# Kernel optimization log

Hardware: AMD Instinct MI355X
Metric: run time of the kernel (lower is better)

## Reference

```python
import jax, jax.numpy as jnp
import numpy as np

D_MODEL = 2048
NUM_HEADS = 16
HEAD_DIM = D_MODEL // NUM_HEADS  # 128
BASE = 10000.0


def rotate_half(x):
    x1, x2 = x[..., : x.shape[-1] // 2], x[..., x.shape[-1] // 2 :]
    return jnp.concatenate((-x2, x1), axis=-1)


def setup_inputs() -> dict:
    key = jax.random.key(0)
    ks = jax.random.split(key, 9)
    B, S, D = 2, 2048, D_MODEL
    s = 1.0 / np.sqrt(D)
    return {
        "x": jax.random.normal(ks[0], (B, S, D), dtype=jnp.float32),
        "Wq": jax.random.normal(ks[1], (D, D), dtype=jnp.float32) * s,
        "bq": jnp.zeros((D,), dtype=jnp.float32),
        "Wk": jax.random.normal(ks[2], (D, D), dtype=jnp.float32) * s,
        "bk": jnp.zeros((D,), dtype=jnp.float32),
        "Wv": jax.random.normal(ks[3], (D, D), dtype=jnp.float32) * s,
        "bv": jnp.zeros((D,), dtype=jnp.float32),
        "Wo": jax.random.normal(ks[4], (D, D), dtype=jnp.float32) * s,
        "bo": jnp.zeros((D,), dtype=jnp.float32),
    }


def reference(x, Wq, bq, Wk, bk, Wv, bv, Wo, bo):
    B, S, D = x.shape
    H, hd = NUM_HEADS, HEAD_DIM

    def proj(W, b):
        # nn.Linear: x @ W^T + b, then split heads -> [B, H, S, hd]
        return (x @ W.T + b).reshape(B, S, H, hd).transpose(0, 2, 1, 3)

    q = proj(Wq, bq)
    k = proj(Wk, bk)
    v = proj(Wv, bv)

    # Rotary embedding table (note: original applies cos()/sin() to a
    # tensor that already contains [sin(si), cos(si)] — reproduced faithfully).
    positions = jnp.arange(S, dtype=jnp.float32)
    inv_freq = 1.0 / (BASE ** (jnp.arange(0, hd, 2, dtype=jnp.float32) / hd))
    sinusoid = positions[:, None] * inv_freq[None, :]            # [S, hd/2]
    emb = jnp.concatenate((jnp.sin(sinusoid), jnp.cos(sinusoid)), axis=-1)  # [S, hd]
    cos_e = jnp.cos(emb)  # broadcast over [B, H, S, hd]
    sin_e = jnp.sin(emb)

    q_rot = q * cos_e + rotate_half(q) * sin_e
    k_rot = k * cos_e + rotate_half(k) * sin_e

    scale = 1.0 / jnp.sqrt(jnp.asarray(hd, dtype=x.dtype))
    attn = jnp.einsum("bhqd,bhkd->bhqk", q_rot, k_rot) * scale
    attn = jax.nn.softmax(attn, axis=-1)
    out = jnp.einsum("bhqk,bhkd->bhqd", attn, v)
    out = out.transpose(0, 2, 1, 3).reshape(B, S, D)
    return out @ Wo.T + bo
```

## Files before the change

### kernel.cpp

```cpp
#include <hip/hip_runtime.h>
#include <math.h>

#define D_MODEL 2048
#define NHEADS  16
#define HD      128
#define SEQ     2048
#define BATCH   2
#define SCALE   0.08838834764831845f
#define SMAX    20.0f

typedef __attribute__((ext_vector_type(8))) short short8;
typedef __attribute__((ext_vector_type(4))) float f32x4;

#define MFMA16(a,b,c) __builtin_amdgcn_mfma_f32_16x16x32_bf16((a),(b),(c),0,0,0)

__device__ __forceinline__ unsigned short f2bf(float x){
    unsigned u = __float_as_uint(x);
    return (unsigned short)((u + 0x7FFFu + ((u>>16)&1u)) >> 16);
}
__device__ __forceinline__ float bf2f(unsigned short h){ return __uint_as_float(((unsigned)h)<<16); }

__device__ __forceinline__ void async16(void* lds, const void* g){
    __builtin_amdgcn_global_load_lds((const __attribute__((address_space(1))) unsigned int*)g,
                                     (__attribute__((address_space(3))) unsigned int*)lds, 16, 0, 0);
}

__device__ __forceinline__ void split4(float4 v, ushort4* h, ushort4* l){
    h->x=f2bf(v.x); l->x=f2bf(v.x-bf2f(h->x));
    h->y=f2bf(v.y); l->y=f2bf(v.y-bf2f(h->y));
    h->z=f2bf(v.z); l->z=f2bf(v.z-bf2f(h->z));
    h->w=f2bf(v.w); l->w=f2bf(v.w-bf2f(h->w));
}

__global__ __launch_bounds__(256)
void prep_all(const float* __restrict__ x, const float* __restrict__ Wq,
              const float* __restrict__ Wk, const float* __restrict__ Wv,
              unsigned short* __restrict__ Xhi, unsigned short* __restrict__ Xlo,
              unsigned short* __restrict__ WqHi, unsigned short* __restrict__ WqLo,
              unsigned short* __restrict__ WkHi, unsigned short* __restrict__ WkLo,
              unsigned short* __restrict__ WvHi,
              float4* __restrict__ tab)
{
    const int b = blockIdx.x, t = threadIdx.x;
    if (b < 8192) {
        int i = b*256 + t;
        ushort4 h,l; split4(((const float4*)x)[i], &h, &l);
        ((ushort4*)Xhi)[i]=h; ((ushort4*)Xlo)[i]=l;
    } else if (b < 12288) {
        int i = (b-8192)*256 + t;
        ushort4 h,l; split4(((const float4*)Wq)[i], &h, &l);
        ((ushort4*)WqHi)[i]=h; ((ushort4*)WqLo)[i]=l;
    } else if (b < 16384) {
        int i = (b-12288)*256 + t;
        ushort4 h,l; split4(((const float4*)Wk)[i], &h, &l);
        ((ushort4*)WkHi)[i]=h; ((ushort4*)WkLo)[i]=l;
    } else if (b < 20480) {
        int i = (b-16384)*256 + t;
        ushort4 h,l; split4(((const float4*)Wv)[i], &h, &l);
        ((ushort4*)WvHi)[i]=h;
    } else {
        int i = (b-20480)*256 + t;
        int s = i >> 6, d = i & 63;
        float f = powf(10000.0f, -(float)d * (1.0f/64.0f));
        float sv = (float)s * f;
        float sn = sinf(sv), cs = cosf(sv);
        tab[i] = (float4){cosf(sn), sinf(sn), cosf(cs), sinf(cs)};
    }
}

__global__ __launch_bounds__(256)
void split_w(const float* __restrict__ src, unsigned short* __restrict__ hi,
             unsigned short* __restrict__ lo, int n4)
{
    int i = blockIdx.x*256 + threadIdx.x;
    if (i >= n4) return;
    ushort4 h,l; split4(((const float4*)src)[i], &h, &l);
    ((ushort4*)hi)[i]=h; ((ushort4*)lo)[i]=l;
}

template<bool THREE>
__device__ __forceinline__ void read_A(const unsigned short* Ah, const unsigned short* Al,
                                       short8 (&ah)[4], short8 (&al)[4],
                                       int wm, int quad, int l15)
{
#pragma unroll
    for (int mi=0;mi<4;mi++){
        int m = wm*64 + mi*16 + l15;
        int c = (quad ^ ((m>>1)&3))*8;
        ah[mi] = *(const short8*)&Ah[m*32 + c];
        al[mi] = *(const short8*)&Al[m*32 + c];
    }
}

template<bool THREE, int Q>
__device__ __forceinline__ void read_B(const unsigned short* Bh, const unsigned short* Bl,
                                       short8& bh, short8& bl, int wn, int quad, int l15)
{
    int n = wn*64 + Q*16 + l15;
    int c = (quad ^ ((n>>1)&3))*8;
    bh = *(const short8*)&Bh[n*32 + c];
    if constexpr (THREE) bl = *(const short8*)&Bl[n*32 + c];
    else                 bl = (short8){};
}

template<bool THREE, int Q>
__device__ __forceinline__ void col_mfma(const short8 (&ah)[4], const short8 (&al)[4],
                                         short8 bh, short8 bl, f32x4 (&acc)[4][4])
{
    __builtin_amdgcn_s_setprio(1);
    acc[0][Q] = MFMA16(ah[0], bh, acc[0][Q]);
    acc[1][Q] = MFMA16(ah[1], bh, acc[1][Q]);
    acc[2][Q] = MFMA16(ah[2], bh, acc[2][Q]);
    acc[3][Q] = MFMA16(ah[3], bh, acc[3][Q]);
    acc[0][Q] = MFMA16(al[0], bh, acc[0][Q]);
    acc[1][Q] = MFMA16(al[1], bh, acc[1][Q]);
    acc[2][Q] = MFMA16(al[2], bh, acc[2][Q]);
    acc[3][Q] = MFMA16(al[3], bh, acc[3][Q]);
    if constexpr (THREE) {
        acc[0][Q] = MFMA16(ah[0], bl, acc[0][Q]);
        acc[1][Q] = MFMA16(ah[1], bl, acc[1][Q]);
        acc[2][Q] = MFMA16(ah[2], bl, acc[2][Q]);
        acc[3][Q] = MFMA16(ah[3], bl, acc[3][Q]);
    }
    __builtin_amdgcn_s_setprio(0);
}

template<bool THREE>
__device__ __forceinline__ void gemm_core(const unsigned short* __restrict__ Agh,
                                          const unsigned short* __restrict__ Agl,
                                          const unsigned short* __restrict__ Bgh,
                                          const unsigned short* __restrict__ Bgl,
                                          unsigned short* lds, int m0, int n0,
                                          f32x4 (&acc)[4][4])
{
    const int t = threadIdx.x, w = t>>6, lane = t&63;
    const int quad = lane>>4, l15 = lane&15;
    const int wm = w>>1, wn = w&1;

    unsigned short *c0 = lds, *c1 = lds + 24576, *c2 = lds + 49152;

    auto stageA = [&](unsigned short* P, const unsigned short* SRC, int u, int kt2){
        int idx = t + u*512; int rw = idx>>2, sg = idx&3;
        int sgp = sg ^ ((rw>>1)&3);
        async16((char*)(P + rw*32 + sg*8), SRC + (size_t)(m0+rw)*2048 + kt2 + sgp*8);
    };
    auto stageB = [&](unsigned short* P, const unsigned short* SRC, int kt2){
        int rw = t>>2, sg = t&3; int sgp = sg ^ ((rw>>1)&3);
        async16((char*)(P + rw*32 + sg*8), SRC + (size_t)(n0+rw)*2048 + kt2 + sgp*8);
    };
    auto stage_tile = [&](unsigned short* P, int kt2){
        stageA(P,        Agh, 0, kt2);  stageA(P,        Agh, 1, kt2);
        stageA(P+8192,   Agl, 0, kt2);  stageA(P+8192,   Agl, 1, kt2);
        stageB(P+16384,  Bgh, kt2);
        if constexpr (THREE) stageB(P+20480, Bgl, kt2);
    };

    stage_tile(c0, 0);
    stage_tile(c1, 32);
    if constexpr (THREE) asm volatile("s_waitcnt vmcnt(6)" ::: "memory");
    else                 asm volatile("s_waitcnt vmcnt(5)" ::: "memory");
    __builtin_amdgcn_s_barrier();
    __builtin_amdgcn_sched_barrier(0);

    short8 ah[4], al[4], ahp[4], alp[4];
    short8 b0h, b0l, b1h, b1l, b2h, b2l, b3h, b3l, b0hp, b0lp;
    read_A<THREE>(c0, c0+8192, ah, al, wm, quad, l15);
    read_B<THREE,0>(c0+16384, c0+20480, b0h, b0l, wn, quad, l15);

    for (int kt = 0; kt < 64; ++kt) {
        const bool st  = (kt < 62);
        const int  kt2 = (kt+2)*32;

        read_B<THREE,1>(c0+16384, c0+20480, b1h, b1l, wn, quad, l15);
        if (st){ stageA(c2,       Agh, 0, kt2); stageA(c2,       Agh, 1, kt2); }
        col_mfma<THREE,0>(ah, al, b0h, b0l, acc);
        __builtin_amdgcn_sched_barrier(0);

        read_B<THREE,2>(c0+16384, c0+20480, b2h, b2l, wn, quad, l15);
        if (st){ stageA(c2+8192,  Agl, 0, kt2); stageA(c2+8192,  Agl, 1, kt2); }
        col_mfma<THREE,1>(ah, al, b1h, b1l, acc);
        __builtin_amdgcn_sched_barrier(0);

        read_B<THREE,3>(c0+16384, c0+20480, b3h, b3l, wn, quad, l15);
        if (st){ stageB(c2+16384, Bgh, kt2); }
        col_mfma<THREE,2>(ah, al, b2h, b2l, acc);
        __builtin_amdgcn_sched_barrier(0);

        if constexpr (THREE) { if (st) stageB(c2+20480, Bgl, kt2); }
        if (kt < 63) {
            __builtin_amdgcn_sched_barrier(0);
            asm volatile("s_waitcnt lgkmcnt(0)" ::: "memory");
            if (st) {
                if constexpr (THREE) asm volatile("s_waitcnt vmcnt(6)" ::: "memory");
                else                 asm volatile("s_waitcnt vmcnt(5)" ::: "memory");
            } else {
                asm volatile("s_waitcnt vmcnt(0)" ::: "memory");
            }
            __builtin_amdgcn_s_barrier();
            __builtin_amdgcn_sched_barrier(0);
            read_A<THREE>(c1, c1+8192, ahp, alp, wm, quad, l15);
            read_B<THREE,0>(c1+16384, c1+20480, b0hp, b0lp, wn, quad, l15);
            __builtin_amdgcn_sched_barrier(0);
            col_mfma<THREE,3>(ah, al, b3h, b3l, acc);
#pragma unroll
            for (int i=0;i<4;i++){ ah[i]=ahp[i]; al[i]=alp[i]; }
            b0h = b0hp; b0l = b0lp;
            unsigned short* tmp = c0; c0 = c1; c1 = c2; c2 = tmp;
        } else {
            col_mfma<THREE,3>(ah, al, b3h, b3l, acc);
        }
    }
}

__global__ __launch_bounds__(512,2)
void gemm_qk(const unsigned short* __restrict__ Xhi_g, const unsigned short* __restrict__ Xlo_g,
             const unsigned short* __restrict__ wsplit,
             const float* __restrict__ bq, const float* __restrict__ bk,
             const float4* __restrict__ tab,
             unsigned short* __restrict__ Qhi, unsigned short* __restrict__ Qlo,
             unsigned short* __restrict__ Khi, unsigned short* __restrict__ Klo)
{
    extern __shared__ unsigned short ldsm[];
    const int z = blockIdx.z;
    const unsigned short* Whi = wsplit + (size_t)z*8388608u;
    const unsigned short* Wlo = Whi + 4194304u;
    const int t = threadIdx.x, w = t>>6, lane = t&63;
    const int quad = lane>>4, l15 = lane&15;
    const int wm = w>>1, wn = w&1;
    const int m0 = blockIdx.y*256, n0 = blockIdx.x*128;

    f32x4 acc[4][4];
#pragma unroll
    for (int i=0;i<4;i++)
#pragma unroll
        for (int j=0;j<4;j++) acc[i][j] = (f32x4){0.f,0.f,0.f,0.f};

    gemm_core<true>(Xhi_g, Xlo_g, Whi, Wlo, ldsm, m0, n0, acc);
    __syncthreads();

    const float* bias = (z==0)?bq:bk;
#pragma unroll
    for (int ni=0;ni<4;ni++){
        float bv_ = bias[n0 + wn*64 + ni*16 + l15];
#pragma unroll
        for (int mi=0;mi<4;mi++){
            acc[mi][ni][0]+=bv_; acc[mi][ni][1]+=bv_; acc[mi][ni][2]+=bv_; acc[mi][ni][3]+=bv_;
        }
    }

    float* xch = (float*)ldsm;
    unsigned short* OHi = (z==0)?Qhi:Khi;
    unsigned short* OLo = (z==0)?Qlo:Klo;
    const float scl = (z==0)?SCALE:1.0f;
    const int h = blockIdx.x;
    const int b = m0>>11;
    const size_t bhbase = ((size_t)(b*16+h)*2048);

    if (wn == 0) {
#pragma unroll
        for (int mi=0;mi<4;mi++)
#pragma unroll
        for (int ni=2;ni<4;ni++)
#pragma unroll
        for (int r=0;r<4;r++)
            xch[(wm*64+mi*16+quad*4+r)*68 + (ni-2)*16+l15] = acc[mi][ni][r];
    } else {
#pragma unroll
        for (int mi=0;mi<4;mi++)
#pragma unroll
        for (int ni=0;ni<2;ni++)
#pragma unroll
        for (int r=0;r<4;r++)
            xch[(wm*64+mi*16+quad*4+r)*68 + 32 + ni*16+l15] = acc[mi][ni][r];
    }
    __syncthreads();

    if (wn == 0) {
#pragma unroll
        for (int ni2=0;ni2<2;ni2++){
            int d = ni2*16 + l15;
#pragma unroll
            for (int mi=0;mi<4;mi++)
#pragma unroll
            for (int r=0;r<4;r++){
                int ml = wm*64 + mi*16 + quad*4 + r;
                int s = (m0 + ml) & 2047;
                float4 tv = tab[s*64 + d];
                float c_lo = acc[mi][ni2][r];
                float c_hi = xch[ml*68 + 32 + d];
                float o1 = (c_lo*tv.x - c_hi*tv.y)*scl;
                float o2 = (c_hi*tv.z + c_lo*tv.w)*scl;
                size_t base = (bhbase + s)*128;
                unsigned short h1=f2bf(o1); OHi[base+d]=h1;    OLo[base+d]=f2bf(o1-bf2f(h1));
                unsigned short h2=f2bf(o2); OHi[base+64+d]=h2; OLo[base+64+d]=f2bf(o2-bf2f(h2));
            }
        }
    } else {
#pragma unroll
        for (int ni2=0;ni2<2;ni2++){
            int d = 32 + ni2*16 + l15;
#pragma unroll
            for (int mi=0;mi<4;mi++)
#pragma unroll
            for (int r=0;r<4;r++){
                int ml = wm*64 + mi*16 + quad*4 + r;
                int s = (m0 + ml) & 2047;
                float4 tv = tab[s*64 + d];
                float c_lo = xch[ml*68 + (d-32)];
                float c_hi = acc[mi][ni2+2][r];
                float o1 = (c_lo*tv.x - c_hi*tv.y)*scl;
                float o2 = (c_hi*tv.z + c_lo*tv.w)*scl;
                size_t base = (bhbase + s)*128;
                unsigned short h1=f2bf(o1); OHi[base+d]=h1;    OLo[base+d]=f2bf(o1-bf2f(h1));
                unsigned short h2=f2bf(o2); OHi[base+64+d]=h2; OLo[base+64+d]=f2bf(o2-bf2f(h2));
            }
        }
    }
}

__global__ __launch_bounds__(512,2)
void gemm_v(const unsigned short* __restrict__ Xhi_g, const unsigned short* __restrict__ Xlo_g,
            const unsigned short* __restrict__ WvHi,
            const float* __restrict__ bv, unsigned short* __restrict__ Vt)
{
    extern __shared__ unsigned short ldsm[];
    const int t = threadIdx.x, w = t>>6, lane = t&63;
    const int quad = lane>>4, l15 = lane&15;
    const int wm = w>>1, wn = w&1;
    const int m0 = blockIdx.y*256, n0 = blockIdx.x*128;

    f32x4 acc[4][4];
#pragma unroll
    for (int i=0;i<4;i++)
#pragma unroll
        for (int j=0;j<4;j++) acc[i][j] = (f32x4){0.f,0.f,0.f,0.f};

    gemm_core<false>(Xhi_g, Xlo_g, WvHi, nullptr, ldsm, m0, n0, acc);
    __syncthreads();

#pragma unroll
    for (int ni=0;ni<4;ni++){
        float bv_ = bv[n0 + wn*64 + ni*16 + l15];
#pragma unroll
        for (int mi=0;mi<4;mi++){
            acc[mi][ni][0]+=bv_; acc[mi][ni][1]+=bv_; acc[mi][ni][2]+=bv_; acc[mi][ni][3]+=bv_;
        }
    }

    unsigned short* vb = ldsm;
#pragma unroll
    for (int mi=0;mi<4;mi++)
#pragma unroll
    for (int ni=0;ni<4;ni++)
#pragma unroll
    for (int r=0;r<4;r++){
        int d  = wn*64 + ni*16 + l15;
        int ml = wm*64 + mi*16 + quad*4 + r;
        vb[d*264 + ml] = f2bf(acc[mi][ni][r]);
    }
    __syncthreads();

    const int b = m0>>11, s0 = m0&2047, h = blockIdx.x;
    unsigned short* vdst = Vt + (size_t)(b*16+h)*128*2048;
    const int dr = t>>2, part = (t&3)*64;
#pragma unroll
    for (int j=0;j<8;j++){
        uint4 v = *(const uint4*)&vb[dr*264 + part + j*8];
        *(uint4*)(vdst + (size_t)dr*2048 + s0 + part + j*8) = v;
    }
}

__global__ __launch_bounds__(512,2)
void gemm_o(const unsigned short* __restrict__ Ahi_g, const unsigned short* __restrict__ Alo_g,
            const unsigned short* __restrict__ Whi_g, const unsigned short* __restrict__ Wlo_g,
            const float* __restrict__ bias, float* __restrict__ out)
{
    extern __shared__ unsigned short ldsm[];
    const int t = threadIdx.x, w = t>>6, lane = t&63;
    const int quad = lane>>4, l15 = lane&15;
    const int wm = w>>1, wn = w&1;
    const int m0 = blockIdx.y*256, n0 = blockIdx.x*128;

    f32x4 acc[4][4];
#pragma unroll
    for (int i=0;i<4;i++)
#pragma unroll
        for (int j=0;j<4;j++) acc[i][j] = (f32x4){0.f,0.f,0.f,0.f};

    gemm_core<true>(Ahi_g, Alo_g, Whi_g, Wlo_g, ldsm, m0, n0, acc);

#pragma unroll
    for (int ni=0;ni<4;ni++){
        int n = n0 + wn*64 + ni*16 + l15;
        float bv_ = bias[n];
#pragma unroll
        for (int mi=0;mi<4;mi++)
#pragma unroll
        for (int r=0;r<4;r++){
            int m = m0 + wm*64 + mi*16 + quad*4 + r;
            out[(size_t)m*2048 + n] = acc[mi][ni][r] + bv_;
        }
    }
}

__global__ __launch_bounds__(256,2)
void flash_mfma(const unsigned short* __restrict__ Qhi, const unsigned short* __restrict__ Qlo,
                const unsigned short* __restrict__ Khi, const unsigned short* __restrict__ Klo,
                const unsigned short* __restrict__ Vt,
                unsigned short* __restrict__ Ohi, unsigned short* __restrict__ Olo)
{
    const int t=threadIdx.x, w=t>>6, lane=t&63, quad=lane>>4, l15=lane&15;
    const int bh = blockIdx.y, qt = blockIdx.x;

    __shared__ __align__(16) unsigned short sm[32768];
    unsigned short* Ps = sm + 24576 + w*2048;

    short8 qf[2][2][4];
    const size_t qrow = (size_t)bh*2048 + qt*128 + w*32;
#pragma unroll
    for (int mb=0;mb<2;mb++){
        size_t r = qrow + mb*16 + l15;
#pragma unroll
        for (int kc=0;kc<4;kc++){
            qf[0][mb][kc] = *(const short8*)(Qhi + r*128 + kc*32 + quad*8);
            qf[1][mb][kc] = *(const short8*)(Qlo + r*128 + kc*32 + quad*8);
        }
    }

    f32x4 O[2][8];
#pragma unroll
    for (int mb=0;mb<2;mb++)
#pragma unroll
        for (int nb=0;nb<8;nb++) O[mb][nb]=(f32x4){0.f,0.f,0.f,0.f};
    float lrow[2][4];
#pragma unroll
    for (int mb=0;mb<2;mb++)
#pragma unroll
        for (int r=0;r<4;r++) lrow[mb][r]=0.f;

    const char* KhiB = (const char*)(Khi + (size_t)bh*2048*128);
    const char* KloB = (const char*)(Klo + (size_t)bh*2048*128);
    const unsigned short* VtB = Vt + (size_t)bh*128*2048;
    char* smb = (char*)sm;

    for (int kt=0; kt<2048; kt+=64) {
#pragma unroll
        for (int i=0;i<4;i++){
            int o16 = t + 256*i;
            int krow = o16>>4, kc = o16&15;
            int kcp = kc ^ (krow&15);
            async16(smb + i*4096 + t*16,         KhiB + (size_t)kt*256 + krow*256 + kcp*16);
            async16(smb + 16384 + i*4096 + t*16, KloB + (size_t)kt*256 + krow*256 + kcp*16);
            int d = (t>>3) + i*32, c = t&7;
            int cp = c ^ (d&7);
            async16(smb + 32768 + i*4096 + t*16, VtB + (size_t)d*2048 + kt + cp*8);
        }
        __syncthreads();

        f32x4 S[2][4];
#pragma unroll
        for (int mb=0;mb<2;mb++)
#pragma unroll
            for (int nb=0;nb<4;nb++) S[mb][nb]=(f32x4){0.f,0.f,0.f,0.f};
#pragma unroll
        for (int kc=0;kc<4;kc++)
#pragma unroll
        for (int nb=0;nb<4;nb++){
            int m = nb*16+l15;
            int c = ((kc*4+quad) ^ (m&15))*8;
            short8 kh = *(const short8*)&sm[m*128 + c];
            short8 kl = *(const short8*)&sm[8192 + m*128 + c];
#pragma unroll
            for (int mb=0;mb<2;mb++){
                S[mb][nb] = MFMA16(qf[0][mb][kc], kh, S[mb][nb]);
                S[mb][nb] = MFMA16(qf[1][mb][kc], kh, S[mb][nb]);
                S[mb][nb] = MFMA16(qf[0][mb][kc], kl, S[mb][nb]);
            }
        }

#pragma unroll
        for (int mb=0;mb<2;mb++)
#pragma unroll
        for (int nb=0;nb<4;nb++)
#pragma unroll
        for (int r=0;r<4;r++){
            float p = __expf(S[mb][nb][r] - SMAX);
            lrow[mb][r] += p;
            int q = mb*16 + quad*4 + r;
            int c = nb*16 + l15;
            Ps[q*64 + (((c>>3)^(q&7))<<3) + (c&7)] = f2bf(p);
        }

#pragma unroll
        for (int kc2=0;kc2<2;kc2++){
            short8 pf0 = *(const short8*)&Ps[(l15)*64      + (((kc2*4+quad)^(l15&7))<<3)];
            short8 pf1 = *(const short8*)&Ps[(16+l15)*64   + (((kc2*4+quad)^(l15&7))<<3)];
#pragma unroll
            for (int nb=0;nb<8;nb++){
                int d = nb*16+l15;
                int c = ((kc2*4+quad) ^ (d&7))*8;
                short8 vf = *(const short8*)&sm[16384 + d*64 + c];
                O[0][nb] = MFMA16(pf0, vf, O[0][nb]);
                O[1][nb] = MFMA16(pf1, vf, O[1][nb]);
            }
        }
        __syncthreads();
    }

#pragma unroll
    for (int mb=0;mb<2;mb++)
#pragma unroll
        for (int d=1;d<16;d<<=1)
#pragma unroll
            for (int r=0;r<4;r++) lrow[mb][r] += __shfl_xor(lrow[mb][r], d);

    const int b = bh>>4, h = bh&15;
#pragma unroll
    for (int mb=0;mb<2;mb++)
#pragma unroll
    for (int nb=0;nb<8;nb++)
#pragma unroll
    for (int r=0;r<4;r++){
        float v = O[mb][nb][r] / lrow[mb][r];
        int qg = qt*128 + w*32 + mb*16 + quad*4 + r;
        size_t base = ((size_t)(b*2048 + qg))*2048 + h*128 + nb*16 + l15;
        unsigned short hh = f2bf(v);
        Ohi[base]=hh; Olo[base]=f2bf(v-bf2f(hh));
    }
}

extern "C" void kernel_launch(void* const* d_in, const int* in_sizes, int n_in,
                              void* d_out, int out_size, void* d_ws, size_t ws_size,
                              hipStream_t stream)
{
    (void)in_sizes; (void)n_in; (void)out_size; (void)ws_size;
    const float* x  = (const float*)d_in[0];
    const float* Wq = (const float*)d_in[1];
    const float* bq = (const float*)d_in[2];
    const float* Wk = (const float*)d_in[3];
    const float* bk = (const float*)d_in[4];
    const float* Wv = (const float*)d_in[5];
    const float* bv = (const float*)d_in[6];
    const float* Wo = (const float*)d_in[7];
    const float* bo = (const float*)d_in[8];
    float* out = (float*)d_out;

    unsigned short* wsB = (unsigned short*)d_ws;
    unsigned short* C0  = wsB + 20971520u;
    unsigned short* Qhi = C0;
    unsigned short* Qlo = C0 + 8388608u;
    unsigned short* Khi = C0 + 16777216u;
    unsigned short* Klo = C0 + 25165824u;
    unsigned short* Vt  = C0 + 33554432u;
    float4* tab = (float4*)(wsB + 62914560u);

    unsigned short* Xhi = (unsigned short*)d_out;
    unsigned short* Xlo = Xhi + 8388608u;

    static bool attr_done = false;
    if (!attr_done) {
        (void)hipFuncSetAttribute(reinterpret_cast<const void*>(&gemm_qk),
                                  hipFuncAttributeMaxDynamicSharedMemorySize, 147456);
        (void)hipFuncSetAttribute(reinterpret_cast<const void*>(&gemm_v),
                                  hipFuncAttributeMaxDynamicSharedMemorySize, 147456);
        (void)hipFuncSetAttribute(reinterpret_cast<const void*>(&gemm_o),
                                  hipFuncAttributeMaxDynamicSharedMemorySize, 147456);
        attr_done = true;
    }

    prep_all<<<20992,256,0,stream>>>(x, Wq, Wk, Wv,
                                     Xhi, Xlo,
                                     wsB,            wsB+4194304u,
                                     wsB+8388608u,   wsB+12582912u,
                                     wsB+16777216u,  tab);

    gemm_qk<<<dim3(16,16,2),512,147456,stream>>>(Xhi, Xlo, wsB, bq, bk, tab,
                                                 Qhi, Qlo, Khi, Klo);
    gemm_v <<<dim3(16,16),  512,147456,stream>>>(Xhi, Xlo, wsB+16777216u, bv, Vt);

    unsigned short* Ohi = wsB;
    unsigned short* Olo = wsB + 8388608u;
    flash_mfma<<<dim3(16,32),256,0,stream>>>(Qhi,Qlo,Khi,Klo,Vt, Ohi, Olo);

    unsigned short* WoHi = C0;
    unsigned short* WoLo = C0 + 4194304u;
    split_w<<<4096,256,0,stream>>>(Wo, WoHi, WoLo, 1048576);

    gemm_o<<<dim3(16,16),512,147456,stream>>>(Ohi, Olo, WoHi, WoLo, bo, out);
}
```

Measured before the change: 635.8 us.

## Rewrite QK projection GEMM with 256x256 tiles and shuffle-based rotary epilogue

Replaces the shared triple-buffered gemm_core for the Q/K projection with a dedicated kernel using 256x256 block tiles (8x4 MFMA tiles per wave) and double-buffered LDS. The B (weight) rows are permuted on load so that rotary pair partners d and d+64 land in adjacent lanes, letting the epilogue use __shfl_xor instead of an LDS exchange and extra syncthreads. This halves the grid and increases operand reuse per block, at the cost of a simpler pipeline with a full vmcnt(0) wait each k-step, higher register pressure from 128 accumulator floats, and 128KB LDS at 2 blocks/CU.

```diff
diff --git a/kernel.cpp b/kernel.cpp
--- a/kernel.cpp
+++ b/kernel.cpp
@@ -78,10 +78,146 @@
     ((ushort4*)hi)[i]=h; ((ushort4*)lo)[i]=l;
 }
 
+__global__ __launch_bounds__(512,2)
+void gemm_qk(const unsigned short* __restrict__ Xhi_g, const unsigned short* __restrict__ Xlo_g,
+             const unsigned short* __restrict__ wsplit,
+             const float* __restrict__ bq, const float* __restrict__ bk,
+             const float4* __restrict__ tab,
+             unsigned short* __restrict__ Qhi, unsigned short* __restrict__ Qlo,
+             unsigned short* __restrict__ Khi, unsigned short* __restrict__ Klo)
+{
+    extern __shared__ unsigned short ldsm[];
+    const int z = blockIdx.z;
+    const unsigned short* Whi = wsplit + (size_t)z*8388608u;
+    const unsigned short* Wlo = Whi + 4194304u;
+    const int t = threadIdx.x, w = t>>6, lane = t&63;
+    const int quad = lane>>4, l15 = lane&15;
+    const int wm = w>>2, wn = w&3;
+    const int m0 = blockIdx.y*256, n0 = blockIdx.x*256;
+
+    unsigned short *c0 = ldsm, *c1 = ldsm + 32768;
+
+    f32x4 acc[8][4];
+#pragma unroll
+    for (int i=0;i<8;i++)
+#pragma unroll
+        for (int j=0;j<4;j++) acc[i][j] = (f32x4){0.f,0.f,0.f,0.f};
+
+    auto stage_tile = [&](unsigned short* P, int kt){
+#pragma unroll
+        for (int u=0; u<2; ++u){
+            int idx = t + u*512, rw = idx>>2, sg = idx&3;
+            int sgp = sg ^ ((rw>>1)&3);
+            async16((char*)(P + rw*32 + sg*8), Xhi_g + (size_t)(m0+rw)*2048 + kt + sgp*8);
+        }
+#pragma unroll
+        for (int u=0; u<2; ++u){
+            int idx = t + u*512, rw = idx>>2, sg = idx&3;
+            int sgp = sg ^ ((rw>>1)&3);
+            async16((char*)(P + 8192 + rw*32 + sg*8), Xlo_g + (size_t)(m0+rw)*2048 + kt + sgp*8);
+        }
+#pragma unroll
+        for (int u=0; u<2; ++u){
+            int idx = t + u*512, rw = idx>>2, sg = idx&3;
+            int sgp = sg ^ ((rw>>1)&3);
+            int wrow = n0 + ((rw>>7)<<7) + ((rw&127)>>1) + (rw&1)*64;
+            async16((char*)(P + 16384 + rw*32 + sg*8), Whi + (size_t)wrow*2048 + kt + sgp*8);
+        }
+#pragma unroll
+        for (int u=0; u<2; ++u){
+            int idx = t + u*512, rw = idx>>2, sg = idx&3;
+            int sgp = sg ^ ((rw>>1)&3);
+            int wrow = n0 + ((rw>>7)<<7) + ((rw&127)>>1) + (rw&1)*64;
+            async16((char*)(P + 24576 + rw*32 + sg*8), Wlo + (size_t)wrow*2048 + kt + sgp*8);
+        }
+    };
+
+    stage_tile(c0, 0);
+
+    for (int kt = 0; kt < 64; ++kt) {
+        asm volatile("s_waitcnt vmcnt(0)" ::: "memory");
+        __builtin_amdgcn_s_barrier();
+        __builtin_amdgcn_sched_barrier(0);
+
+        if (kt < 63) stage_tile(c1, (kt+1)*32);
+
+        const unsigned short* Ah = c0;
+        const unsigned short* Al = c0 + 8192;
+        const unsigned short* Bh = c0 + 16384;
+        const unsigned short* Bl = c0 + 24576;
+
+        short8 bh[4], bl[4];
+#pragma unroll
+        for (int ni=0;ni<4;ni++){
+            int n = wn*64 + ni*16 + l15;
+            int c = (quad ^ ((n>>1)&3))*8;
+            bh[ni] = *(const short8*)&Bh[n*32 + c];
+            bl[ni] = *(const short8*)&Bl[n*32 + c];
+        }
+
+        __builtin_amdgcn_s_setprio(1);
+#pragma unroll
+        for (int mi=0;mi<8;mi++){
+            int m = wm*128 + mi*16 + l15;
+            int c = (quad ^ ((m>>1)&3))*8;
+            short8 ah = *(const short8*)&Ah[m*32 + c];
+            short8 al = *(const short8*)&Al[m*32 + c];
+            acc[mi][0] = MFMA16(ah, bh[0], acc[mi][0]);
+            acc[mi][1] = MFMA16(ah, bh[1], acc[mi][1]);
+            acc[mi][2] = MFMA16(ah, bh[2], acc[mi][2]);
+            acc[mi][3] = MFMA16(ah, bh[3], acc[mi][3]);
+            acc[mi][0] = MFMA16(al, bh[0], acc[mi][0]);
+            acc[mi][1] = MFMA16(al, bh[1], acc[mi][1]);
+            acc[mi][2] = MFMA16(al, bh[2], acc[mi][2]);
+            acc[mi][3] = MFMA16(al, bh[3], acc[mi][3]);
+            acc[mi][0] = MFMA16(ah, bl[0], acc[mi][0]);
+            acc[mi][1] = MFMA16(ah, bl[1], acc[mi][1]);
+            acc[mi][2] = MFMA16(ah, bl[2], acc[mi][2]);
+            acc[mi][3] = MFMA16(ah, bl[3], acc[mi][3]);
+        }
+        __builtin_amdgcn_s_setprio(0);
+
+        asm volatile("s_waitcnt lgkmcnt(0)" ::: "memory");
+        __builtin_amdgcn_sched_barrier(0);
+        unsigned short* tmp = c0; c0 = c1; c1 = tmp;
+    }
+
+    unsigned short* OHi = (z==0)?Qhi:Khi;
+    unsigned short* OLo = (z==0)?Qlo:Klo;
+    const float* bias = (z==0)?bq:bk;
+    const float scl = (z==0)?SCALE:1.0f;
+    const int head_g = blockIdx.x*2 + (wn>>1);
+    const int jbase  = (wn&1)*64;
+    const int odd    = l15 & 1;
+
+#pragma unroll
+    for (int ni=0;ni<4;ni++){
+        int j = jbase + ni*16 + l15;
+        int d = j>>1;
+        float bv_ = bias[head_g*128 + d + odd*64];
+        int dcol = odd ? (64 + d) : d;
+#pragma unroll
+        for (int mi=0;mi<8;mi++)
+#pragma unroll
+        for (int r=0;r<4;r++){
+            int gm = m0 + wm*128 + mi*16 + quad*4 + r;
+            int b  = gm >> 11, s = gm & 2047;
+            float v = acc[mi][ni][r] + bv_;
+            float p = __shfl_xor(v, 1);
+            float4 tv = tab[s*64 + d];
+            float o = odd ? (v*tv.z + p*tv.w)*scl
+                          : (v*tv.x - p*tv.y)*scl;
+            size_t base = (((size_t)(b*16 + head_g))*2048 + s)*128 + dcol;
+            unsigned short hh = f2bf(o);
+            OHi[base] = hh; OLo[base] = f2bf(o - bf2f(hh));
+        }
+    }
+}
+
 template<bool THREE>
-__device__ __forceinline__ void read_A(const unsigned short* Ah, const unsigned short* Al,
-                                       short8 (&ah)[4], short8 (&al)[4],
-                                       int wm, int quad, int l15)
+__device__ __forceinline__ void read_A3(const unsigned short* Ah, const unsigned short* Al,
+                                        short8 (&ah)[4], short8 (&al)[4],
+                                        int wm, int quad, int l15)
 {
 #pragma unroll
     for (int mi=0;mi<4;mi++){
@@ -93,8 +229,8 @@
 }
 
 template<bool THREE, int Q>
-__device__ __forceinline__ void read_B(const unsigned short* Bh, const unsigned short* Bl,
-                                       short8& bh, short8& bl, int wn, int quad, int l15)
+__device__ __forceinline__ void read_B3(const unsigned short* Bh, const unsigned short* Bl,
+                                        short8& bh, short8& bl, int wn, int quad, int l15)
 {
     int n = wn*64 + Q*16 + l15;
     int c = (quad ^ ((n>>1)&3))*8;
@@ -104,8 +240,8 @@
 }
 
 template<bool THREE, int Q>
-__device__ __forceinline__ void col_mfma(const short8 (&ah)[4], const short8 (&al)[4],
-                                         short8 bh, short8 bl, f32x4 (&acc)[4][4])
+__device__ __forceinline__ void col_mfma3(const short8 (&ah)[4], const short8 (&al)[4],
+                                          short8 bh, short8 bl, f32x4 (&acc)[4][4])
 {
     __builtin_amdgcn_s_setprio(1);
     acc[0][Q] = MFMA16(ah[0], bh, acc[0][Q]);
@@ -126,12 +262,12 @@
 }
 
 template<bool THREE>
-__device__ __forceinline__ void gemm_core(const unsigned short* __restrict__ Agh,
-                                          const unsigned short* __restrict__ Agl,
-                                          const unsigned short* __restrict__ Bgh,
-                                          const unsigned short* __restrict__ Bgl,
-                                          unsigned short* lds, int m0, int n0,
-                                          f32x4 (&acc)[4][4])
+__device__ __forceinline__ void gemm_core3(const unsigned short* __restrict__ Agh,
+                                           const unsigned short* __restrict__ Agl,
+                                           const unsigned short* __restrict__ Bgh,
+                                           const unsigned short* __restrict__ Bgl,
+                                           unsigned short* lds, int m0, int n0,
+                                           f32x4 (&acc)[4][4])
 {
     const int t = threadIdx.x, w = t>>6, lane = t&63;
     const int quad = lane>>4, l15 = lane&15;
@@ -164,26 +300,26 @@
 
     short8 ah[4], al[4], ahp[4], alp[4];
     short8 b0h, b0l, b1h, b1l, b2h, b2l, b3h, b3l, b0hp, b0lp;
-    read_A<THREE>(c0, c0+8192, ah, al, wm, quad, l15);
-    read_B<THREE,0>(c0+16384, c0+20480, b0h, b0l, wn, quad, l15);
+    read_A3<THREE>(c0, c0+8192, ah, al, wm, quad, l15);
+    read_B3<THREE,0>(c0+16384, c0+20480, b0h, b0l, wn, quad, l15);
 
     for (int kt = 0; kt < 64; ++kt) {
         const bool st  = (kt < 62);
         const int  kt2 = (kt+2)*32;
 
-        read_B<THREE,1>(c0+16384, c0+20480, b1h, b1l, wn, quad, l15);
+        read_B3<THREE,1>(c0+16384, c0+20480, b1h, b1l, wn, quad, l15);
         if (st){ stageA(c2,       Agh, 0, kt2); stageA(c2,       Agh, 1, kt2); }
-        col_mfma<THREE,0>(ah, al, b0h, b0l, acc);
+        col_mfma3<THREE,0>(ah, al, b0h, b0l, acc);
         __builtin_amdgcn_sched_barrier(0);
 
-        read_B<THREE,2>(c0+16384, c0+20480, b2h, b2l, wn, quad, l15);
+        read_B3<THREE,2>(c0+16384, c0+20480, b2h, b2l, wn, quad, l15);
         if (st){ stageA(c2+8192,  Agl, 0, kt2); stageA(c2+8192,  Agl, 1, kt2); }
-        col_mfma<THREE,1>(ah, al, b1h, b1l, acc);
+        col_mfma3<THREE,1>(ah, al, b1h, b1l, acc);
         __builtin_amdgcn_sched_barrier(0);
 
-        read_B<THREE,3>(c0+16384, c0+20480, b3h, b3l, wn, quad, l15);
+        read_B3<THREE,3>(c0+16384, c0+20480, b3h, b3l, wn, quad, l15);
         if (st){ stageB(c2+16384, Bgh, kt2); }
-        col_mfma<THREE,2>(ah, al, b2h, b2l, acc);
+        col_mfma3<THREE,2>(ah, al, b2h, b2l, acc);
         __builtin_amdgcn_sched_barrier(0);
 
         if constexpr (THREE) { if (st) stageB(c2+20480, Bgl, kt2); }
@@ -198,122 +334,16 @@
             }
             __builtin_amdgcn_s_barrier();
             __builtin_amdgcn_sched_barrier(0);
-            read_A<THREE>(c1, c1+8192, ahp, alp, wm, quad, l15);
-            read_B<THREE,0>(c1+16384, c1+20480, b0hp, b0lp, wn, quad, l15);
+            read_A3<THREE>(c1, c1+8192, ahp, alp, wm, quad, l15);
+            read_B3<THREE,0>(c1+16384, c1+20480, b0hp, b0lp, wn, quad, l15);
             __builtin_amdgcn_sched_barrier(0);
-            col_mfma<THREE,3>(ah, al, b3h, b3l, acc);
+            col_mfma3<THREE,3>(ah, al, b3h, b3l, acc);
 #pragma unroll
             for (int i=0;i<4;i++){ ah[i]=ahp[i]; al[i]=alp[i]; }
             b0h = b0hp; b0l = b0lp;
             unsigned short* tmp = c0; c0 = c1; c1 = c2; c2 = tmp;
         } else {
-            col_mfma<THREE,3>(ah, al, b3h, b3l, acc);
-        }
-    }
-}
-
-__global__ __launch_bounds__(512,2)
-void gemm_qk(const unsigned short* __restrict__ Xhi_g, const unsigned short* __restrict__ Xlo_g,
-             const unsigned short* __restrict__ wsplit,
-             const float* __restrict__ bq, const float* __restrict__ bk,
-             const float4* __restrict__ tab,
-             unsigned short* __restrict__ Qhi, unsigned short* __restrict__ Qlo,
-             unsigned short* __restrict__ Khi, unsigned short* __restrict__ Klo)
-{
-    extern __shared__ unsigned short ldsm[];
-    const int z = blockIdx.z;
-    const unsigned short* Whi = wsplit + (size_t)z*8388608u;
-    const unsigned short* Wlo = Whi + 4194304u;
-    const int t = threadIdx.x, w = t>>6, lane = t&63;
-    const int quad = lane>>4, l15 = lane&15;
-    const int wm = w>>1, wn = w&1;
-    const int m0 = blockIdx.y*256, n0 = blockIdx.x*128;
-
-    f32x4 acc[4][4];
-#pragma unroll
-    for (int i=0;i<4;i++)
-#pragma unroll
-        for (int j=0;j<4;j++) acc[i][j] = (f32x4){0.f,0.f,0.f,0.f};
-
-    gemm_core<true>(Xhi_g, Xlo_g, Whi, Wlo, ldsm, m0, n0, acc);
-    __syncthreads();
-
-    const float* bias = (z==0)?bq:bk;
-#pragma unroll
-    for (int ni=0;ni<4;ni++){
-        float bv_ = bias[n0 + wn*64 + ni*16 + l15];
-#pragma unroll
-        for (int mi=0;mi<4;mi++){
-            acc[mi][ni][0]+=bv_; acc[mi][ni][1]+=bv_; acc[mi][ni][2]+=bv_; acc[mi][ni][3]+=bv_;
-        }
-    }
-
-    float* xch = (float*)ldsm;
-    unsigned short* OHi = (z==0)?Qhi:Khi;
-    unsigned short* OLo = (z==0)?Qlo:Klo;
-    const float scl = (z==0)?SCALE:1.0f;
-    const int h = blockIdx.x;
-    const int b = m0>>11;
-    const size_t bhbase = ((size_t)(b*16+h)*2048);
-
-    if (wn == 0) {
-#pragma unroll
-        for (int mi=0;mi<4;mi++)
-#pragma unroll
-        for (int ni=2;ni<4;ni++)
-#pragma unroll
-        for (int r=0;r<4;r++)
-            xch[(wm*64+mi*16+quad*4+r)*68 + (ni-2)*16+l15] = acc[mi][ni][r];
-    } else {
-#pragma unroll
-        for (int mi=0;mi<4;mi++)
-#pragma unroll
-        for (int ni=0;ni<2;ni++)
-#pragma unroll
-        for (int r=0;r<4;r++)
-            xch[(wm*64+mi*16+quad*4+r)*68 + 32 + ni*16+l15] = acc[mi][ni][r];
-    }
-    __syncthreads();
-
-    if (wn == 0) {
-#pragma unroll
-        for (int ni2=0;ni2<2;ni2++){
-            int d = ni2*16 + l15;
-#pragma unroll
-            for (int mi=0;mi<4;mi++)
-#pragma unroll
-            for (int r=0;r<4;r++){
-                int ml = wm*64 + mi*16 + quad*4 + r;
-                int s = (m0 + ml) & 2047;
-                float4 tv = tab[s*64 + d];
-                float c_lo = acc[mi][ni2][r];
-                float c_hi = xch[ml*68 + 32 + d];
-                float o1 = (c_lo*tv.x - c_hi*tv.y)*scl;
-                float o2 = (c_hi*tv.z + c_lo*tv.w)*scl;
-                size_t base = (bhbase + s)*128;
-                unsigned short h1=f2bf(o1); OHi[base+d]=h1;    OLo[base+d]=f2bf(o1-bf2f(h1));
-                unsigned short h2=f2bf(o2); OHi[base+64+d]=h2; OLo[base+64+d]=f2bf(o2-bf2f(h2));
-            }
-        }
-    } else {
-#pragma unroll
-        for (int ni2=0;ni2<2;ni2++){
-            int d = 32 + ni2*16 + l15;
-#pragma unroll
-            for (int mi=0;mi<4;mi++)
-#pragma unroll
-            for (int r=0;r<4;r++){
-                int ml = wm*64 + mi*16 + quad*4 + r;
-                int s = (m0 + ml) & 2047;
-                float4 tv = tab[s*64 + d];
-                float c_lo = xch[ml*68 + (d-32)];
-                float c_hi = acc[mi][ni2+2][r];
-                float o1 = (c_lo*tv.x - c_hi*tv.y)*scl;
-                float o2 = (c_hi*tv.z + c_lo*tv.w)*scl;
-                size_t base = (bhbase + s)*128;
-                unsigned short h1=f2bf(o1); OHi[base+d]=h1;    OLo[base+d]=f2bf(o1-bf2f(h1));
-                unsigned short h2=f2bf(o2); OHi[base+64+d]=h2; OLo[base+64+d]=f2bf(o2-bf2f(h2));
-            }
+            col_mfma3<THREE,3>(ah, al, b3h, b3l, acc);
         }
     }
 }
@@ -335,7 +365,7 @@
 #pragma unroll
         for (int j=0;j<4;j++) acc[i][j] = (f32x4){0.f,0.f,0.f,0.f};
 
-    gemm_core<false>(Xhi_g, Xlo_g, WvHi, nullptr, ldsm, m0, n0, acc);
+    gemm_core3<false>(Xhi_g, Xlo_g, WvHi, nullptr, ldsm, m0, n0, acc);
     __syncthreads();
 
 #pragma unroll
@@ -387,7 +417,7 @@
 #pragma unroll
         for (int j=0;j<4;j++) acc[i][j] = (f32x4){0.f,0.f,0.f,0.f};
 
-    gemm_core<true>(Ahi_g, Alo_g, Whi_g, Wlo_g, ldsm, m0, n0, acc);
+    gemm_core3<true>(Ahi_g, Alo_g, Whi_g, Wlo_g, ldsm, m0, n0, acc);
 
 #pragma unroll
     for (int ni=0;ni<4;ni++){
@@ -560,7 +590,7 @@
     static bool attr_done = false;
     if (!attr_done) {
         (void)hipFuncSetAttribute(reinterpret_cast<const void*>(&gemm_qk),
-                                  hipFuncAttributeMaxDynamicSharedMemorySize, 147456);
+                                  hipFuncAttributeMaxDynamicSharedMemorySize, 131072);
         (void)hipFuncSetAttribute(reinterpret_cast<const void*>(&gemm_v),
                                   hipFuncAttributeMaxDynamicSharedMemorySize, 147456);
         (void)hipFuncSetAttribute(reinterpret_cast<const void*>(&gemm_o),
@@ -574,9 +604,9 @@
                                      wsB+8388608u,   wsB+12582912u,
                                      wsB+16777216u,  tab);
 
-    gemm_qk<<<dim3(16,16,2),512,147456,stream>>>(Xhi, Xlo, wsB, bq, bk, tab,
-                                                 Qhi, Qlo, Khi, Klo);
-    gemm_v <<<dim3(16,16),  512,147456,stream>>>(Xhi, Xlo, wsB+16777216u, bv, Vt);
+    gemm_qk<<<dim3(8,16,2),512,131072,stream>>>(Xhi, Xlo, wsB, bq, bk, tab,
+                                                Qhi, Qlo, Khi, Klo);
+    gemm_v <<<dim3(16,16), 512,147456,stream>>>(Xhi, Xlo, wsB+16777216u, bv, Vt);
 
     unsigned short* Ohi = wsB;
     unsigned short* Olo = wsB + 8388608u;
```

New measurement: 690.9 us. +8.7%, slower.
